# Kernel tuning notes

Measured on AMD Instinct MI355X. Metric: run time of the kernel, lower is better.

The kernel has to match this reference:

```python
import jax, jax.numpy as jnp
import numpy as np

NEG_INF = -1e30  # stand-in for float('-inf') that is safe in fp16/bf16 softmax


def setup_inputs() -> dict:
    key = jax.random.key(0)
    ks = jax.random.split(key, 5)
    B, S, D, E, H = 2, 2048, 1024, 8, 4096  # H = 4*D per Expert MLP
    scale = 0.02
    return {
        "x": jax.random.normal(ks[0], (B, S, D), dtype=jnp.float32),
        "router_w": jax.random.normal(ks[1], (D, E), dtype=jnp.float32) * scale,
        "router_b": jnp.zeros((E,), dtype=jnp.float32),
        "w1": jax.random.normal(ks[2], (E, D, H), dtype=jnp.float32) * scale,
        "b1": jnp.zeros((E, H), dtype=jnp.float32),
        "w2": jax.random.normal(ks[3], (E, H, D), dtype=jnp.float32) * scale,
        "b2": jnp.zeros((E, D), dtype=jnp.float32),
    }


def _moe_forward(x, router_w, router_b, w1, b1, w2, b2, top_k=2):
    B, S, D = x.shape
    E = router_w.shape[1]
    # --- TopkRouter ---
    logits = jnp.einsum("bsd,de->bse", x, router_w) + router_b      # [B,S,E]
    top_vals, top_idx = jax.lax.top_k(logits, top_k)                  # [B,S,k]
    # scatter top-k logits into a -inf tensor == mask non-topk to -inf
    keep = (jax.nn.one_hot(top_idx, E, dtype=logits.dtype).sum(-2) > 0)
    sparse_logits = jnp.where(keep, logits, NEG_INF)
    gating = jax.nn.softmax(sparse_logits, axis=-1)                   # [B,S,E], 0 off top-k

    # --- Experts: dense grouped MLP; gating is exactly 0 for non-selected
    # experts, so weighting by gating reproduces the masked gather/scatter loop.
    xf = x.reshape(-1, D)                                             # [T,D]
    gf = gating.reshape(-1, E)                                        # [T,E]
    h = jax.nn.relu(jnp.einsum("td,edh->eth", xf, w1) + b1[:, None, :])  # [E,T,H]
    y = jnp.einsum("eth,ehd->etd", h, w2) + b2[:, None, :]            # [E,T,D]
    out = jnp.einsum("etd,te->td", y, gf)                             # combine
    return out.reshape(B, S, D)


def reference(x, router_w, router_b, w1, b1, w2, b2):
    return _moe_forward(x, router_w, router_b, w1, b1, w2, b2, top_k=2)
```

## Files before the change

kernel.cpp:

```cpp
#include <hip/hip_runtime.h>
#include <stdint.h>

typedef float f32x4 __attribute__((ext_vector_type(4)));
typedef short s16x8 __attribute__((ext_vector_type(8)));
typedef unsigned short u16x4 __attribute__((ext_vector_type(4)));
typedef unsigned short u16x8 __attribute__((ext_vector_type(8)));

__device__ __forceinline__ unsigned short f2bf(float f) {
  union { float f; unsigned u; } v; v.f = f;
  unsigned r = v.u + 0x7fffu + ((v.u >> 16) & 1u);
  return (unsigned short)(r >> 16);
}

__device__ __forceinline__ float bf2f(unsigned short u) {
  union { unsigned u; float f; } v; v.u = ((unsigned)u) << 16;
  return v.f;
}

__device__ __forceinline__ void gld_lds16(const void* g, void* l) {
  __builtin_amdgcn_global_load_lds(
      (__attribute__((address_space(1))) void*)(void*)g,
      (__attribute__((address_space(3))) void*)l,
      16, 0, 0);
}

__device__ __forceinline__ double shfl_xor_dbl(double v, int m) {
  long long l = __double_as_longlong(v);
  int lo = (int)(l & 0xffffffffLL), hi = (int)(l >> 32);
  lo = __shfl_xor(lo, m, 64);
  hi = __shfl_xor(hi, m, 64);
  return __longlong_as_double(((long long)hi << 32) | (unsigned)lo);
}

__device__ __forceinline__ int padded_base(const int* counts, int e) {
  int s = 0;
#pragma unroll
  for (int i = 0; i < 8; ++i) {
    int c = (counts[i] + 127) & ~127;
    s += (i < e) ? c : 0;
  }
  return s;
}

__global__ __launch_bounds__(256) void k_transpose_cvt(
    const float* __restrict__ src, unsigned short* __restrict__ dst, int R, int C) {
  __shared__ float tile[64][65];
  const size_t RC = (size_t)R * C;
  const float* s = src + (size_t)blockIdx.z * RC;
  unsigned short* d = dst + (size_t)blockIdx.z * RC;
  int r0 = blockIdx.y * 64, c0 = blockIdx.x * 64;
  int tid = threadIdx.x;
#pragma unroll
  for (int i = 0; i < 4; ++i) {
    int slot = tid + i * 256;
    int r = slot >> 4, c4 = (slot & 15) << 2;
    float4 v = *(const float4*)(s + (size_t)(r0 + r) * C + c0 + c4);
    tile[r][c4 + 0] = v.x; tile[r][c4 + 1] = v.y;
    tile[r][c4 + 2] = v.z; tile[r][c4 + 3] = v.w;
  }
  __syncthreads();
#pragma unroll
  for (int i = 0; i < 2; ++i) {
    int slot = tid + i * 256;
    int c = slot >> 3, r8 = (slot & 7) << 3;
    u16x8 o;
#pragma unroll
    for (int j = 0; j < 8; ++j) o[j] = f2bf(tile[r8 + j][c]);
    *(u16x8*)(d + (size_t)(c0 + c) * R + r0 + r8) = o;
  }
}

__global__ __launch_bounds__(256) void k_router(
    const float* __restrict__ x, const float* __restrict__ rw,
    const float* __restrict__ rb, unsigned short* __restrict__ xb,
    int* __restrict__ counts, uint2* __restrict__ lists, int T, int D) {
  int lane = threadIdx.x & 63;
  int wid = (int)((blockIdx.x * blockDim.x + threadIdx.x) >> 6);
  int nw = (int)((gridDim.x * blockDim.x) >> 6);
  for (int t = wid; t < T; t += nw) {
    double acc[8] = {0, 0, 0, 0, 0, 0, 0, 0};
    for (int j = lane * 4; j < D; j += 256) {
      float4 xv = *(const float4*)(x + (size_t)t * D + j);
      u16x4 o;
      o[0] = f2bf(xv.x); o[1] = f2bf(xv.y); o[2] = f2bf(xv.z); o[3] = f2bf(xv.w);
      *(u16x4*)(xb + (size_t)t * D + j) = o;
      float xs[4] = {xv.x, xv.y, xv.z, xv.w};
#pragma unroll
      for (int q = 0; q < 4; ++q) {
        const float* rp = rw + (size_t)(j + q) * 8;
#pragma unroll
        for (int e = 0; e < 8; ++e) acc[e] += (double)xs[q] * (double)rp[e];
      }
    }
#pragma unroll
    for (int e = 0; e < 8; ++e) {
#pragma unroll
      for (int off = 32; off >= 1; off >>= 1) acc[e] += shfl_xor_dbl(acc[e], off);
    }
    if (lane == 0) {
      double v0 = -1e300, v1 = -1e300; int e0 = 0, e1 = 0;
#pragma unroll
      for (int e = 0; e < 8; ++e) {
        double v = acc[e] + (double)rb[e];
        if (v > v0) { v1 = v0; e1 = e0; v0 = v; e0 = e; }
        else if (v > v1) { v1 = v; e1 = e; }
      }
      double ex = exp(v1 - v0);
      float g0 = (float)(1.0 / (1.0 + ex));
      float g1 = (float)(ex / (1.0 + ex));
      int s0 = atomicAdd(&counts[e0], 1);
      int s1 = atomicAdd(&counts[e1], 1);
      lists[(size_t)e0 * T + s0] = make_uint2((unsigned)t, __float_as_uint(g0));
      lists[(size_t)e1 * T + s1] = make_uint2((unsigned)t | 0x80000000u, __float_as_uint(g1));
    }
  }
}

__global__ __launch_bounds__(256, 4) void k_gemm1(
    const unsigned short* __restrict__ xb, const unsigned short* __restrict__ w1bT,
    const float* __restrict__ b1, const int* __restrict__ counts,
    const uint2* __restrict__ lists,
    unsigned short* __restrict__ he, int T, int D, int H) {
  int e = blockIdx.z;
  int cnt = counts[e];
  int nwg = gridDim.x * gridDim.y;
  int flat = blockIdx.y * gridDim.x + blockIdx.x;
  int idx = (flat & 7) * (nwg >> 3) + (flat >> 3);
  int bn = idx / gridDim.y, bm = idx - bn * gridDim.y;
  int m0 = bm * 128;
  if (m0 >= cnt) return;
  int n0 = bn * 128;
  int baseE = padded_base(counts, e);
  int tid = threadIdx.x;

  __shared__ __align__(16) unsigned short As[128 * 64];
  __shared__ __align__(16) unsigned short Bs[128 * 64];

  const uint2* le = lists + (size_t)e * T;
  const unsigned short* srcA[4];
  const unsigned short* srcB[4];
#pragma unroll
  for (int i = 0; i < 4; ++i) {
    int row = (tid >> 3) + i * 32;
    int mrow = m0 + row; if (mrow > cnt - 1) mrow = cnt - 1;
    unsigned tok = le[mrow].x & 0x7fffffffu;
    int G = (tid & 7) ^ (row & 7);
    srcA[i] = xb + (size_t)tok * D + G * 8;
    srcB[i] = w1bT + ((size_t)e * H + n0 + row) * D + G * 8;
  }

  int lane = tid & 63;
  int wr = tid >> 7, wc = (tid >> 6) & 1;
  int lrow = lane & 15, lgrp = (lane >> 4) & 3;
  int mb = wr * 64, nb = wc * 64;
  int rsw = lrow & 7;

  f32x4 acc[4][4];
#pragma unroll
  for (int a = 0; a < 4; ++a)
#pragma unroll
    for (int b = 0; b < 4; ++b) acc[a][b] = (f32x4){0.f, 0.f, 0.f, 0.f};

  int nk = D >> 6;
  for (int kt = 0; kt < nk; ++kt) {
#pragma unroll
    for (int i = 0; i < 4; ++i) {
      gld_lds16(srcA[i], As + tid * 8 + i * 2048);
      gld_lds16(srcB[i], Bs + tid * 8 + i * 2048);
      srcA[i] += 64;
      srcB[i] += 64;
    }
    asm volatile("s_waitcnt vmcnt(0)" ::: "memory");
    __syncthreads();
#pragma unroll
    for (int ks = 0; ks < 2; ++ks) {
      s16x8 av[4], bv[4];
#pragma unroll
      for (int mf = 0; mf < 4; ++mf) {
        int row = mb + mf * 16 + lrow;
        int Gp = (ks * 4 + lgrp) ^ rsw;
        av[mf] = *(const s16x8*)(As + row * 64 + Gp * 8);
      }
#pragma unroll
      for (int nf = 0; nf < 4; ++nf) {
        int row = nb + nf * 16 + lrow;
        int Gp = (ks * 4 + lgrp) ^ rsw;
        bv[nf] = *(const s16x8*)(Bs + row * 64 + Gp * 8);
      }
#pragma unroll
      for (int mf = 0; mf < 4; ++mf)
#pragma unroll
        for (int nf = 0; nf < 4; ++nf)
          acc[mf][nf] = __builtin_amdgcn_mfma_f32_16x16x32_bf16(av[mf], bv[nf], acc[mf][nf], 0, 0, 0);
    }
    __syncthreads();
  }

#pragma unroll
  for (int nf = 0; nf < 4; ++nf) {
    int n = nb + nf * 16 + lrow;
    float b1v = b1[(size_t)e * H + n0 + n];
#pragma unroll
    for (int mf = 0; mf < 4; ++mf) {
      f32x4 v = acc[mf][nf];
#pragma unroll
      for (int j = 0; j < 4; ++j) {
        int gm = m0 + mb + mf * 16 + lgrp * 4 + j;
        float val = v[j] + b1v;
        val = val > 0.f ? val : 0.f;
        he[((size_t)baseE + gm) * H + n0 + n] = f2bf(val);
      }
    }
  }
}

__global__ __launch_bounds__(256, 4) void k_gemm2(
    const unsigned short* __restrict__ he, const unsigned short* __restrict__ w2bT,
    const float* __restrict__ b2, const int* __restrict__ counts,
    const uint2* __restrict__ lists,
    unsigned short* __restrict__ y, int T, int H, int D) {
  int z = blockIdx.z;
  int e = z >> 1, ksp = z & 1;
  int cnt = counts[e];
  int nwg = gridDim.x * gridDim.y;
  int flat = blockIdx.y * gridDim.x + blockIdx.x;
  int idx = (flat & 7) * (nwg >> 3) + (flat >> 3);
  int bn = idx / gridDim.y, bm = idx - bn * gridDim.y;
  int m0 = bm * 128;
  if (m0 >= cnt) return;
  int n0 = bn * 128;
  int baseE = padded_base(counts, e);
  int tid = threadIdx.x;
  int koff = ksp * (H >> 1);

  __shared__ __align__(16) unsigned short As[128 * 64];
  __shared__ __align__(16) unsigned short Bs[128 * 64];

  const uint2* le = lists + (size_t)e * T;
  const unsigned short* srcA[4];
  const unsigned short* srcB[4];
#pragma unroll
  for (int i = 0; i < 4; ++i) {
    int row = (tid >> 3) + i * 32;
    int G = (tid & 7) ^ (row & 7);
    srcA[i] = he + ((size_t)baseE + m0 + row) * H + koff + G * 8;
    srcB[i] = w2bT + ((size_t)e * D + n0 + row) * H + koff + G * 8;
  }

  int lane = tid & 63;
  int wr = tid >> 7, wc = (tid >> 6) & 1;
  int lrow = lane & 15, lgrp = (lane >> 4) & 3;
  int mb = wr * 64, nb = wc * 64;
  int rsw = lrow & 7;

  f32x4 acc[4][4];
#pragma unroll
  for (int a = 0; a < 4; ++a)
#pragma unroll
    for (int b = 0; b < 4; ++b) acc[a][b] = (f32x4){0.f, 0.f, 0.f, 0.f};

  int nk = H >> 7;
  for (int kt = 0; kt < nk; ++kt) {
#pragma unroll
    for (int i = 0; i < 4; ++i) {
      gld_lds16(srcA[i], As + tid * 8 + i * 2048);
      gld_lds16(srcB[i], Bs + tid * 8 + i * 2048);
      srcA[i] += 64;
      srcB[i] += 64;
    }
    asm volatile("s_waitcnt vmcnt(0)" ::: "memory");
    __syncthreads();
#pragma unroll
    for (int ks = 0; ks < 2; ++ks) {
      s16x8 av[4], bv[4];
#pragma unroll
      for (int mf = 0; mf < 4; ++mf) {
        int row = mb + mf * 16 + lrow;
        int Gp = (ks * 4 + lgrp) ^ rsw;
        av[mf] = *(const s16x8*)(As + row * 64 + Gp * 8);
      }
#pragma unroll
      for (int nf = 0; nf < 4; ++nf) {
        int row = nb + nf * 16 + lrow;
        int Gp = (ks * 4 + lgrp) ^ rsw;
        bv[nf] = *(const s16x8*)(Bs + row * 64 + Gp * 8);
      }
#pragma unroll
      for (int mf = 0; mf < 4; ++mf)
#pragma unroll
        for (int nf = 0; nf < 4; ++nf)
          acc[mf][nf] = __builtin_amdgcn_mfma_f32_16x16x32_bf16(av[mf], bv[nf], acc[mf][nf], 0, 0, 0);
    }
    __syncthreads();
  }

  float b2v[4];
#pragma unroll
  for (int nf = 0; nf < 4; ++nf)
    b2v[nf] = (ksp == 0) ? b2[(size_t)e * D + n0 + nb + nf * 16 + lrow] : 0.f;

#pragma unroll
  for (int mf = 0; mf < 4; ++mf) {
#pragma unroll
    for (int j = 0; j < 4; ++j) {
      int gm = m0 + mb + mf * 16 + lgrp * 4 + j;
      if (gm < cnt) {
        uint2 en = le[gm];
        unsigned tok = en.x & 0x7fffffffu;
        unsigned rank = en.x >> 31;
        float g = __uint_as_float(en.y);
        unsigned short* yrow = y + (((size_t)(rank * 2 + ksp)) * T + tok) * D + n0;
#pragma unroll
        for (int nf = 0; nf < 4; ++nf)
          yrow[nb + nf * 16 + lrow] = f2bf((acc[mf][nf][j] + b2v[nf]) * g);
      }
    }
  }
}

__global__ __launch_bounds__(256) void k_combine(
    const unsigned short* __restrict__ y, float* __restrict__ out, size_t n8) {
  size_t i = (size_t)blockIdx.x * 256 + threadIdx.x;
  size_t stride = (size_t)gridDim.x * 256;
  size_t n = n8 * 8;
  for (; i < n8; i += stride) {
    s16x8 a = *(const s16x8*)(y + i * 8);
    s16x8 b = *(const s16x8*)(y + n + i * 8);
    s16x8 c = *(const s16x8*)(y + 2 * n + i * 8);
    s16x8 d = *(const s16x8*)(y + 3 * n + i * 8);
    float r[8];
#pragma unroll
    for (int j = 0; j < 8; ++j)
      r[j] = bf2f((unsigned short)a[j]) + bf2f((unsigned short)b[j]) +
             bf2f((unsigned short)c[j]) + bf2f((unsigned short)d[j]);
    float4* o = (float4*)(out + i * 8);
    o[0] = make_float4(r[0], r[1], r[2], r[3]);
    o[1] = make_float4(r[4], r[5], r[6], r[7]);
  }
}

extern "C" void kernel_launch(void* const* d_in, const int* in_sizes, int n_in,
                              void* d_out, int out_size, void* d_ws, size_t ws_size,
                              hipStream_t stream) {
  const float* x  = (const float*)d_in[0];
  const float* rw = (const float*)d_in[1];
  const float* rb = (const float*)d_in[2];
  const float* w1 = (const float*)d_in[3];
  const float* b1 = (const float*)d_in[4];
  const float* w2 = (const float*)d_in[5];
  const float* b2 = (const float*)d_in[6];
  float* out = (float*)d_out;

  int E = in_sizes[2];
  int D = in_sizes[1] / E;
  int H = in_sizes[4] / E;
  int T = in_sizes[0] / D;

  char* ws = (char*)d_ws;
  size_t off = 0;
  auto alloc = [&](size_t bytes) -> void* {
    void* p = ws + off;
    off = (off + bytes + 255) & ~(size_t)255;
    return p;
  };
  unsigned short* xb   = (unsigned short*)alloc((size_t)T * D * 2);
  unsigned short* w1bT = (unsigned short*)alloc((size_t)E * D * H * 2);
  unsigned short* w2bT = (unsigned short*)alloc((size_t)E * D * H * 2);
  unsigned short* he   = (unsigned short*)alloc(((size_t)2 * T + E * 128) * H * 2);
  unsigned short* y    = (unsigned short*)alloc((size_t)4 * T * D * 2);
  int* counts          = (int*)alloc(64);
  uint2* lists         = (uint2*)alloc((size_t)E * T * 8);

  hipMemsetAsync(counts, 0, 64, stream);

  dim3 b256(256);
  k_router<<<dim3(256), b256, 0, stream>>>(x, rw, rb, xb, counts, lists, T, D);
  k_transpose_cvt<<<dim3(D / 64, H / 64, E), b256, 0, stream>>>(w2, w2bT, H, D);
  k_transpose_cvt<<<dim3(H / 64, D / 64, E), b256, 0, stream>>>(w1, w1bT, D, H);

  int mt = (T + 127) / 128;
  k_gemm1<<<dim3(H / 128, mt, E), b256, 0, stream>>>(xb, w1bT, b1, counts, lists, he, T, D, H);
  k_gemm2<<<dim3(D / 128, mt, E * 2), b256, 0, stream>>>(he, w2bT, b2, counts, lists, y, T, H, D);

  size_t n8 = (size_t)T * D / 8;
  k_combine<<<dim3(2048), b256, 0, stream>>>(y, out, n8);
}
```

Before: 400.9 us.

## Widen gemm2 tile to 128x256 with 512 threads and merge weight transposes

```diff
diff --git a/kernel.cpp b/kernel.cpp
--- a/kernel.cpp
+++ b/kernel.cpp
@@ -42,14 +42,22 @@
   return s;
 }
 
-__global__ __launch_bounds__(256) void k_transpose_cvt(
-    const float* __restrict__ src, unsigned short* __restrict__ dst, int R, int C) {
+__global__ __launch_bounds__(256) void k_transpose_cvt2(
+    const float* __restrict__ w1, const float* __restrict__ w2,
+    unsigned short* __restrict__ w1bT, unsigned short* __restrict__ w2bT,
+    int D, int H) {
+  int z = blockIdx.y;
+  int e = z & 7;
+  bool is_w1 = z >= 8;
+  int R = is_w1 ? D : H, C = is_w1 ? H : D;
+  const size_t RC = (size_t)R * C;
+  const float* s = (is_w1 ? w1 : w2) + (size_t)e * RC;
+  unsigned short* d = (is_w1 ? w1bT : w2bT) + (size_t)e * RC;
+  int tpc = C >> 6;
+  int bx = blockIdx.x % tpc, by = blockIdx.x / tpc;
+  int r0 = by * 64, c0 = bx * 64;
+  int tid = threadIdx.x;
   __shared__ float tile[64][65];
-  const size_t RC = (size_t)R * C;
-  const float* s = src + (size_t)blockIdx.z * RC;
-  unsigned short* d = dst + (size_t)blockIdx.z * RC;
-  int r0 = blockIdx.y * 64, c0 = blockIdx.x * 64;
-  int tid = threadIdx.x;
 #pragma unroll
   for (int i = 0; i < 4; ++i) {
     int slot = tid + i * 256;
@@ -214,7 +222,7 @@
   }
 }
 
-__global__ __launch_bounds__(256, 4) void k_gemm2(
+__global__ __launch_bounds__(512, 4) void k_gemm2(
     const unsigned short* __restrict__ he, const unsigned short* __restrict__ w2bT,
     const float* __restrict__ b2, const int* __restrict__ counts,
     const uint2* __restrict__ lists,
@@ -228,27 +236,33 @@
   int bn = idx / gridDim.y, bm = idx - bn * gridDim.y;
   int m0 = bm * 128;
   if (m0 >= cnt) return;
-  int n0 = bn * 128;
+  int n0 = bn * 256;
   int baseE = padded_base(counts, e);
   int tid = threadIdx.x;
   int koff = ksp * (H >> 1);
 
   __shared__ __align__(16) unsigned short As[128 * 64];
-  __shared__ __align__(16) unsigned short Bs[128 * 64];
+  __shared__ __align__(16) unsigned short Bs[256 * 64];
 
   const uint2* le = lists + (size_t)e * T;
-  const unsigned short* srcA[4];
+  const unsigned short* srcA[2];
   const unsigned short* srcB[4];
 #pragma unroll
-  for (int i = 0; i < 4; ++i) {
-    int row = (tid >> 3) + i * 32;
+  for (int i = 0; i < 2; ++i) {
+    int row = (tid >> 3) + i * 64;
     int G = (tid & 7) ^ (row & 7);
     srcA[i] = he + ((size_t)baseE + m0 + row) * H + koff + G * 8;
+  }
+#pragma unroll
+  for (int i = 0; i < 4; ++i) {
+    int row = (tid >> 3) + i * 64;
+    int G = (tid & 7) ^ (row & 7);
     srcB[i] = w2bT + ((size_t)e * D + n0 + row) * H + koff + G * 8;
   }
 
   int lane = tid & 63;
-  int wr = tid >> 7, wc = (tid >> 6) & 1;
+  int w = tid >> 6;
+  int wr = w >> 2, wc = w & 3;
   int lrow = lane & 15, lgrp = (lane >> 4) & 3;
   int mb = wr * 64, nb = wc * 64;
   int rsw = lrow & 7;
@@ -262,10 +276,13 @@
   int nk = H >> 7;
   for (int kt = 0; kt < nk; ++kt) {
 #pragma unroll
+    for (int i = 0; i < 2; ++i) {
+      gld_lds16(srcA[i], As + tid * 8 + i * 4096);
+      srcA[i] += 64;
+    }
+#pragma unroll
     for (int i = 0; i < 4; ++i) {
-      gld_lds16(srcA[i], As + tid * 8 + i * 2048);
-      gld_lds16(srcB[i], Bs + tid * 8 + i * 2048);
-      srcA[i] += 64;
+      gld_lds16(srcB[i], Bs + tid * 8 + i * 4096);
       srcB[i] += 64;
     }
     asm volatile("s_waitcnt vmcnt(0)" ::: "memory");
@@ -373,14 +390,14 @@
 
   hipMemsetAsync(counts, 0, 64, stream);
 
-  dim3 b256(256);
+  dim3 b256(256), b512(512);
   k_router<<<dim3(256), b256, 0, stream>>>(x, rw, rb, xb, counts, lists, T, D);
-  k_transpose_cvt<<<dim3(D / 64, H / 64, E), b256, 0, stream>>>(w2, w2bT, H, D);
-  k_transpose_cvt<<<dim3(H / 64, D / 64, E), b256, 0, stream>>>(w1, w1bT, D, H);
+  k_transpose_cvt2<<<dim3((D / 64) * (H / 64), 2 * E), b256, 0, stream>>>(
+      w1, w2, w1bT, w2bT, D, H);
 
   int mt = (T + 127) / 128;
   k_gemm1<<<dim3(H / 128, mt, E), b256, 0, stream>>>(xb, w1bT, b1, counts, lists, he, T, D, H);
-  k_gemm2<<<dim3(D / 128, mt, E * 2), b256, 0, stream>>>(he, w2bT, b2, counts, lists, y, T, H, D);
+  k_gemm2<<<dim3(D / 256, mt, E * 2), b512, 0, stream>>>(he, w2bT, b2, counts, lists, y, T, H, D);
 
   size_t n8 = (size_t)T * D / 8;
   k_combine<<<dim3(2048), b256, 0, stream>>>(y, out, n8);
```

Result: slower. 473.0 us (+18.0%).
